# Kernel tuning notes

Hardware: AMD Instinct MI355X
Metric: run time of the kernel (lower is better)

## Reference

```python
import jax, jax.numpy as jnp
import numpy as np

DIM = 768
NUM_HEADS = 12
HEAD_DIM = DIM // NUM_HEADS
SCALE = HEAD_DIM ** -0.5
B, N = 8, 1024


def setup_inputs() -> dict:
    key = jax.random.key(0)
    k1, k2, k3, k4, k5 = jax.random.split(key, 5)
    x = jax.random.normal(k1, (B, N, DIM), dtype=jnp.float32)
    # qkv: Linear(dim, 3*dim, bias=False); proj: Linear(dim, dim) with bias
    w_qkv = jax.random.normal(k2, (3 * DIM, DIM), dtype=jnp.float32) * (DIM ** -0.5)
    w_proj = jax.random.normal(k3, (DIM, DIM), dtype=jnp.float32) * (DIM ** -0.5)
    b_proj = jnp.zeros((DIM,), dtype=jnp.float32)
    # learned attention mask parameter, shape (H, L, L) with L >= N
    att_mask = jax.random.normal(k4, (NUM_HEADS, N, N), dtype=jnp.float32)
    return {"x": x, "w_qkv": w_qkv, "w_proj": w_proj, "b_proj": b_proj, "att_mask": att_mask}


def reference(x, w_qkv, w_proj, b_proj, att_mask):
    Bx, Nx, C = x.shape
    # qkv projection -> (3, B, H, N, head_dim)
    qkv = (x @ w_qkv.T).reshape(Bx, Nx, 3, NUM_HEADS, C // NUM_HEADS)
    qkv = jnp.transpose(qkv, (2, 0, 3, 1, 4))
    q, k, v = qkv[0], qkv[1], qkv[2]  # gpd_ratio==active_ratio==1 -> scaling factor 1
    # scores [B, H, N, N]
    attn = jnp.einsum('bhnd,bhmd->bhnm', q, k) * SCALE
    # custom sigmoid mask gating before softmax (broadcast over batch)
    attn = attn * jax.nn.sigmoid(att_mask[:, :Nx, :Nx])[None, :, :, :]
    attn = jax.nn.softmax(attn, axis=-1)
    out = jnp.einsum('bhnm,bhmd->bhnd', attn, v)
    out = jnp.transpose(out, (0, 2, 1, 3)).reshape(Bx, Nx, C)
    return out @ w_proj.T + b_proj
```

## Files before the change

kernel.cpp:

```cpp
#include <hip/hip_runtime.h>
#include <math.h>
#include <stdint.h>

typedef unsigned short u16;
typedef __attribute__((ext_vector_type(8))) short short8;
typedef __attribute__((ext_vector_type(4))) float f32x4;

#define GATE_SCALE 0.18033688011112042f

#if __has_builtin(__builtin_amdgcn_exp2f)
#define FEXP2(x) __builtin_amdgcn_exp2f(x)
#else
#define FEXP2(x) exp2f(x)
#endif

__device__ __forceinline__ u16 f2b(float f) {
    union { float f; unsigned u; } v; v.f = f;
    unsigned r = v.u + 0x7fffu + ((v.u >> 16) & 1u);
    return (u16)(r >> 16);
}
__device__ __forceinline__ u16 f2b_hu(float f) {
    union { float f; unsigned u; } v; v.f = f;
    return (u16)((v.u + 0x8000u) >> 16);
}
__device__ __forceinline__ float b2f(u16 u) {
    union { float f; unsigned u; } v; v.u = ((unsigned)u) << 16; return v.f;
}

#define GLL16(gsrc, ldsbase) __builtin_amdgcn_global_load_lds(                    \
    (__attribute__((address_space(1))) void*)(uintptr_t)(gsrc),                   \
    (__attribute__((address_space(3))) void*)(uint32_t)(uintptr_t)(ldsbase),      \
    16, 0, 0)

#define NX4  1572864
#define NW14 442368
#define NW24 147456
#define NXW4 (NX4 + NW14 + NW24)

__global__ __launch_bounds__(256) void prep_xw(
    const float4* __restrict__ x, const float4* __restrict__ wq,
    const float4* __restrict__ wp,
    ushort4* __restrict__ xb, ushort4* __restrict__ wqb,
    ushort4* __restrict__ wpb)
{
    size_t i = (size_t)blockIdx.x * 256 + threadIdx.x;
    float4 v; ushort4* dst; size_t j;
    if (i < NX4)            { j = i;               v = x[j];  dst = xb;  }
    else if (i < NX4 + NW14){ j = i - NX4;         v = wq[j]; dst = wqb; }
    else                    { j = i - (NX4 + NW14);v = wp[j]; dst = wpb; }
    ushort4 o; o.x = f2b(v.x); o.y = f2b(v.y); o.z = f2b(v.z); o.w = f2b(v.w);
    dst[j] = o;
}

__global__ __launch_bounds__(256) void prep_gate(
    const float* __restrict__ mask, u16* __restrict__ gp)
{
    const int bid = blockIdx.x;
    const int h = bid >> 8, qt = (bid >> 4) & 15, kt = bid & 15;
    const int t = threadIdx.x, l = t & 63, w = t >> 6;
    const int fq = l >> 4, fr = l & 15;
    const float* mb = mask + ((size_t)h * 1024 + qt * 64 + 16 * w + 4 * fq) * 1024
                           + kt * 64 + fr;
    union { u16 u[16]; float4 f[2]; } vals;
    #pragma unroll
    for (int i = 0; i < 4; ++i)
        #pragma unroll
        for (int nt = 0; nt < 4; ++nt) {
            float m = mb[(size_t)i * 1024 + nt * 16];
            vals.u[i * 4 + nt] = f2b(GATE_SCALE / (1.f + __expf(-m)));
        }
    float4* dst = (float4*)(gp + (size_t)bid * 4096 + (w * 64 + l) * 16);
    dst[0] = vals.f[0];
    dst[1] = vals.f[1];
}

__global__ __launch_bounds__(256) void qkv_gemm(
    const u16* __restrict__ xb, const u16* __restrict__ wb,
    u16* __restrict__ qb, u16* __restrict__ kb, u16* __restrict__ vb)
{
    __shared__ u16 As[2][4096];
    __shared__ u16 Bs[2][4096];
    const int t = threadIdx.x, l = t & 63, w = t >> 6;
    const int wm = (w & 1) * 64, wn = (w >> 1) * 64;
    const int m0 = blockIdx.y * 128, c0 = blockIdx.x * 128;

    f32x4 acc[4][4];
    #pragma unroll
    for (int i = 0; i < 4; ++i)
        #pragma unroll
        for (int j = 0; j < 4; ++j) { f32x4 z = {0.f,0.f,0.f,0.f}; acc[i][j] = z; }

    const int srow = l >> 2, sseg = l & 3;
    const int gcol = ((sseg ^ (srow & 3)) << 3);
    const u16* a0 = xb + (size_t)(m0 + w * 16 + srow) * 768 + gcol;
    const u16* a1 = a0 + (size_t)64 * 768;
    const u16* b0p = wb + (size_t)(c0 + w * 16 + srow) * 768 + gcol;
    const u16* b1p = b0p + (size_t)64 * 768;
    const int wofs = w * 512;

    const int fr = l & 15, fq = l >> 4;
    const int fseg = (fq ^ (fr & 3)) << 3;

    GLL16(a0, &As[0][wofs]);
    GLL16(a1, &As[0][2048 + wofs]);
    GLL16(b0p, &Bs[0][wofs]);
    GLL16(b1p, &Bs[0][2048 + wofs]);

    for (int kt = 0; kt < 24; ++kt) {
        __syncthreads();
        if (kt < 23) {
            const int kn = (kt + 1) * 32;
            const int nb = (kt + 1) & 1;
            GLL16(a0 + kn, &As[nb][wofs]);
            GLL16(a1 + kn, &As[nb][2048 + wofs]);
            GLL16(b0p + kn, &Bs[nb][wofs]);
            GLL16(b1p + kn, &Bs[nb][2048 + wofs]);
        }
        const u16* A = As[kt & 1];
        const u16* B = Bs[kt & 1];
        short8 af[4], bf[4];
        #pragma unroll
        for (int mt = 0; mt < 4; ++mt)
            af[mt] = *(const short8*)&A[(wm + mt * 16 + fr) * 32 + fseg];
        #pragma unroll
        for (int nt = 0; nt < 4; ++nt)
            bf[nt] = *(const short8*)&B[(wn + nt * 16 + fr) * 32 + fseg];
        #pragma unroll
        for (int mt = 0; mt < 4; ++mt)
            #pragma unroll
            for (int nt = 0; nt < 4; ++nt)
                acc[mt][nt] = __builtin_amdgcn_mfma_f32_16x16x32_bf16(
                    af[mt], bf[nt], acc[mt][nt], 0, 0, 0);
    }

    const int b = m0 >> 10;
    const int n0 = m0 & 1023;
    #pragma unroll
    for (int nt = 0; nt < 4; ++nt) {
        const int c = c0 + wn + nt * 16 + fr;
        const int which = c / 768;
        const int rem = c - which * 768;
        const int h = rem >> 6, d = rem & 63;
        if (which < 2) {
            u16* dst = ((which == 0) ? qb : kb)
                       + ((size_t)(b * 12 + h) * 1024) * 64 + d;
            #pragma unroll
            for (int mt = 0; mt < 4; ++mt)
                #pragma unroll
                for (int r = 0; r < 4; ++r) {
                    const int n = n0 + wm + mt * 16 + fq * 4 + r;
                    dst[(size_t)n * 64] = f2b(acc[mt][nt][r]);
                }
        } else {
            u16* dst = vb + ((size_t)(b * 12 + h) * 64 + d) * 1024
                          + n0 + wm + fq * 4;
            #pragma unroll
            for (int mt = 0; mt < 4; ++mt) {
                ushort4 pk;
                pk.x = f2b(acc[mt][nt][0]); pk.y = f2b(acc[mt][nt][1]);
                pk.z = f2b(acc[mt][nt][2]); pk.w = f2b(acc[mt][nt][3]);
                *(ushort4*)(dst + mt * 16) = pk;
            }
        }
    }
}

__global__ __launch_bounds__(256) void flash_attn(
    const u16* __restrict__ qb, const u16* __restrict__ kb,
    const u16* __restrict__ vt, const u16* __restrict__ gperm,
    u16* __restrict__ aob)
{
    __shared__ u16 Qs[4096], Ks[2][4096], Vts[2][4096], Ps[4096];
    const int t = threadIdx.x, l = t & 63, w = t >> 6;
    const int bid = blockIdx.x;
    const int h = bid >> 7, qt = (bid >> 3) & 15, b = bid & 7;
    const int q0 = qt * 64;
    const u16* hq = qb + (size_t)(b * 12 + h) * 65536;
    const u16* hk = kb + (size_t)(b * 12 + h) * 65536;
    const u16* hv = vt + (size_t)(b * 12 + h) * 65536;
    const u16* hg = gperm + (size_t)(h * 256 + qt * 16) * 4096 + (w * 64 + l) * 16;

    const int sr = l >> 3, ss = l & 7;
    const int sg = ((ss ^ (sr & 7)) << 3);
    const int j0 = w * 2, j1 = w * 2 + 1;

    GLL16(hq + (size_t)(q0 + j0 * 8 + sr) * 64 + sg, Qs + j0 * 512);
    GLL16(hq + (size_t)(q0 + j1 * 8 + sr) * 64 + sg, Qs + j1 * 512);
    GLL16(hk + (size_t)(j0 * 8 + sr) * 64 + sg, &Ks[0][j0 * 512]);
    GLL16(hk + (size_t)(j1 * 8 + sr) * 64 + sg, &Ks[0][j1 * 512]);
    GLL16(hv + (size_t)(j0 * 8 + sr) * 1024 + sg, &Vts[0][j0 * 512]);
    GLL16(hv + (size_t)(j1 * 8 + sr) * 1024 + sg, &Vts[0][j1 * 512]);

    short8 g0 = *(const short8*)(hg);
    short8 g1 = *(const short8*)(hg + 8);

    float l_part[4] = {0.f, 0.f, 0.f, 0.f};
    f32x4 o[4];
    #pragma unroll
    for (int nt = 0; nt < 4; ++nt) { f32x4 z = {0.f,0.f,0.f,0.f}; o[nt] = z; }

    const int fq = l >> 4, fr = l & 15;
    const int sega = ((fq ^ (fr & 7)) << 3);
    const int segb = (((4 + fq) ^ (fr & 7)) << 3);

    for (int kt = 0; kt < 16; ++kt) {
        __syncthreads();
        if (kt < 15) {
            const int nb = (kt + 1) & 1;
            const size_t ko = (size_t)(kt + 1) * 64;
            GLL16(hk + (ko + j0 * 8 + sr) * 64 + sg, &Ks[nb][j0 * 512]);
            GLL16(hk + (ko + j1 * 8 + sr) * 64 + sg, &Ks[nb][j1 * 512]);
            GLL16(hv + (size_t)(j0 * 8 + sr) * 1024 + ko + sg, &Vts[nb][j0 * 512]);
            GLL16(hv + (size_t)(j1 * 8 + sr) * 1024 + ko + sg, &Vts[nb][j1 * 512]);
        }
        const int ktn = (kt < 15) ? kt + 1 : 15;
        short8 gn0 = *(const short8*)(hg + (size_t)ktn * 4096);
        short8 gn1 = *(const short8*)(hg + (size_t)ktn * 4096 + 8);

        const u16* Kc = Ks[kt & 1];
        const u16* Vc = Vts[kt & 1];

        short8 aq0 = *(const short8*)&Qs[(16 * w + fr) * 64 + sega];
        short8 aq1 = *(const short8*)&Qs[(16 * w + fr) * 64 + segb];
        f32x4 sv[4];
        #pragma unroll
        for (int nt = 0; nt < 4; ++nt) {
            short8 k0f = *(const short8*)&Kc[(nt * 16 + fr) * 64 + sega];
            short8 k1f = *(const short8*)&Kc[(nt * 16 + fr) * 64 + segb];
            f32x4 z = {0.f,0.f,0.f,0.f};
            z = __builtin_amdgcn_mfma_f32_16x16x32_bf16(aq0, k0f, z, 0, 0, 0);
            z = __builtin_amdgcn_mfma_f32_16x16x32_bf16(aq1, k1f, z, 0, 0, 0);
            sv[nt] = z;
        }

        #pragma unroll
        for (int i = 0; i < 4; ++i) {
            const int pr = 4 * fq + i;
            #pragma unroll
            for (int nt = 0; nt < 4; ++nt) {
                const int idx = i * 4 + nt;
                const float g = b2f((u16)(idx < 8 ? g0[idx] : g1[idx - 8]));
                const float p = FEXP2(sv[nt][i] * g);
                l_part[i] += p;
                const int col = nt * 16 + fr;
                Ps[w * 1024 + pr * 64 + (((col >> 3) ^ (pr & 7)) << 3) + (col & 7)]
                    = f2b_hu(p);
            }
        }

        short8 ap0 = *(const short8*)&Ps[w * 1024 + fr * 64 + sega];
        short8 ap1 = *(const short8*)&Ps[w * 1024 + fr * 64 + segb];
        #pragma unroll
        for (int nt = 0; nt < 4; ++nt) {
            short8 v0 = *(const short8*)&Vc[(nt * 16 + fr) * 64 + sega];
            short8 v1 = *(const short8*)&Vc[(nt * 16 + fr) * 64 + segb];
            o[nt] = __builtin_amdgcn_mfma_f32_16x16x32_bf16(ap0, v0, o[nt], 0, 0, 0);
            o[nt] = __builtin_amdgcn_mfma_f32_16x16x32_bf16(ap1, v1, o[nt], 0, 0, 0);
        }

        g0 = gn0;
        g1 = gn1;
    }

    float l_i[4];
    #pragma unroll
    for (int i = 0; i < 4; ++i) {
        float s = l_part[i];
        s += __shfl_xor(s, 1, 16);
        s += __shfl_xor(s, 2, 16);
        s += __shfl_xor(s, 4, 16);
        s += __shfl_xor(s, 8, 16);
        l_i[i] = s;
    }

    #pragma unroll
    for (int i = 0; i < 4; ++i) {
        const float inv = 1.f / l_i[i];
        const int n = q0 + 16 * w + 4 * fq + i;
        const size_t rowoff = ((size_t)b * 1024 + n) * 768 + h * 64;
        #pragma unroll
        for (int nt = 0; nt < 4; ++nt)
            aob[rowoff + nt * 16 + fr] = f2b(o[nt][i] * inv);
    }
}

__global__ __launch_bounds__(256) void proj_gemm(
    const u16* __restrict__ aob, const u16* __restrict__ wb,
    const float* __restrict__ bproj, float* __restrict__ out)
{
    __shared__ u16 As[2][4096];
    __shared__ u16 Bs[2][4096];
    const int t = threadIdx.x, l = t & 63, w = t >> 6;
    const int wm = (w & 1) * 64, wn = (w >> 1) * 64;
    const int m0 = blockIdx.y * 128, c0 = blockIdx.x * 128;

    f32x4 acc[4][4];
    #pragma unroll
    for (int i = 0; i < 4; ++i)
        #pragma unroll
        for (int j = 0; j < 4; ++j) { f32x4 z = {0.f,0.f,0.f,0.f}; acc[i][j] = z; }

    const int srow = l >> 2, sseg = l & 3;
    const int gcol = ((sseg ^ (srow & 3)) << 3);
    const u16* a0 = aob + (size_t)(m0 + w * 16 + srow) * 768 + gcol;
    const u16* a1 = a0 + (size_t)64 * 768;
    const u16* b0p = wb + (size_t)(c0 + w * 16 + srow) * 768 + gcol;
    const u16* b1p = b0p + (size_t)64 * 768;
    const int wofs = w * 512;

    const int fr = l & 15, fq = l >> 4;
    const int fseg = (fq ^ (fr & 3)) << 3;

    GLL16(a0, &As[0][wofs]);
    GLL16(a1, &As[0][2048 + wofs]);
    GLL16(b0p, &Bs[0][wofs]);
    GLL16(b1p, &Bs[0][2048 + wofs]);

    for (int kt = 0; kt < 24; ++kt) {
        __syncthreads();
        if (kt < 23) {
            const int kn = (kt + 1) * 32;
            const int nb = (kt + 1) & 1;
            GLL16(a0 + kn, &As[nb][wofs]);
            GLL16(a1 + kn, &As[nb][2048 + wofs]);
            GLL16(b0p + kn, &Bs[nb][wofs]);
            GLL16(b1p + kn, &Bs[nb][2048 + wofs]);
        }
        const u16* A = As[kt & 1];
        const u16* B = Bs[kt & 1];
        short8 af[4], bf[4];
        #pragma unroll
        for (int mt = 0; mt < 4; ++mt)
            af[mt] = *(const short8*)&A[(wm + mt * 16 + fr) * 32 + fseg];
        #pragma unroll
        for (int nt = 0; nt < 4; ++nt)
            bf[nt] = *(const short8*)&B[(wn + nt * 16 + fr) * 32 + fseg];
        #pragma unroll
        for (int mt = 0; mt < 4; ++mt)
            #pragma unroll
            for (int nt = 0; nt < 4; ++nt)
                acc[mt][nt] = __builtin_amdgcn_mfma_f32_16x16x32_bf16(
                    af[mt], bf[nt], acc[mt][nt], 0, 0, 0);
    }

    #pragma unroll
    for (int nt = 0; nt < 4; ++nt) {
        const int c = c0 + wn + nt * 16 + fr;
        const float bias = bproj[c];
        #pragma unroll
        for (int mt = 0; mt < 4; ++mt)
            #pragma unroll
            for (int r = 0; r < 4; ++r) {
                const int m = m0 + wm + mt * 16 + fq * 4 + r;
                out[(size_t)m * 768 + c] = acc[mt][nt][r] + bias;
            }
    }
}

extern "C" void kernel_launch(void* const* d_in, const int* in_sizes, int n_in,
                              void* d_out, int out_size, void* d_ws, size_t ws_size,
                              hipStream_t stream)
{
    const float* x     = (const float*)d_in[0];
    const float* wqkv  = (const float*)d_in[1];
    const float* wproj = (const float*)d_in[2];
    const float* bproj = (const float*)d_in[3];
    const float* mask  = (const float*)d_in[4];
    float* out = (float*)d_out;

    char* ws = (char*)d_ws;
    u16* gperm  = (u16*)(ws);
    u16* xb     = (u16*)(ws + 25165824);
    u16* wqkvb  = (u16*)(ws + 37748736);
    u16* wprojb = (u16*)(ws + 41287680);
    u16* qb     = (u16*)(ws + 42467328);
    u16* kb     = (u16*)(ws + 55050240);
    u16* vb     = (u16*)(ws + 67633152);
    u16* aob    = (u16*)(ws + 80216064);

    prep_xw<<<NXW4 / 256, 256, 0, stream>>>(
        (const float4*)x, (const float4*)wqkv, (const float4*)wproj,
        (ushort4*)xb, (ushort4*)wqkvb, (ushort4*)wprojb);

    prep_gate<<<3072, 256, 0, stream>>>(mask, gperm);

    qkv_gemm<<<dim3(18, 64), 256, 0, stream>>>(xb, wqkvb, qb, kb, vb);

    flash_attn<<<1536, 256, 0, stream>>>(qb, kb, vb, gperm, aob);

    proj_gemm<<<dim3(6, 64), 256, 0, stream>>>(aob, wprojb, bproj, out);
}
```

Before: 249.1 us.

## Use 32x32x16 MFMA with 128-row query tiles in flash attention

The attention kernel now gives each block 128 query rows, so each wave owns 32 rows. It uses 32x32x16 bf16 MFMA instructions in place of 16x16x32, and keeps Q fragments in registers for the whole loop. The gate-permutation prep kernel is rewritten to match the new fragment layout. K/V double buffering is removed in favour of a single buffer with two barriers per iteration, and the kernel sets launch bounds for 3 blocks per CU. This halves the K/V reloads per query and uses larger MFMAs, at the cost of less load/compute overlap and higher register pressure.

```diff
diff --git a/kernel.cpp b/kernel.cpp
--- a/kernel.cpp
+++ b/kernel.cpp
@@ -5,6 +5,7 @@
 typedef unsigned short u16;
 typedef __attribute__((ext_vector_type(8))) short short8;
 typedef __attribute__((ext_vector_type(4))) float f32x4;
+typedef __attribute__((ext_vector_type(16))) float f32x16;
 
 #define GATE_SCALE 0.18033688011112042f
 
@@ -56,22 +57,22 @@
     const float* __restrict__ mask, u16* __restrict__ gp)
 {
     const int bid = blockIdx.x;
-    const int h = bid >> 8, qt = (bid >> 4) & 15, kt = bid & 15;
+    const int kt = bid & 15, qt = (bid >> 4) & 7, h = bid >> 7;
     const int t = threadIdx.x, l = t & 63, w = t >> 6;
-    const int fq = l >> 4, fr = l & 15;
-    const float* mb = mask + ((size_t)h * 1024 + qt * 64 + 16 * w + 4 * fq) * 1024
-                           + kt * 64 + fr;
-    union { u16 u[16]; float4 f[2]; } vals;
-    #pragma unroll
-    for (int i = 0; i < 4; ++i)
-        #pragma unroll
-        for (int nt = 0; nt < 4; ++nt) {
-            float m = mb[(size_t)i * 1024 + nt * 16];
-            vals.u[i * 4 + nt] = f2b(GATE_SCALE / (1.f + __expf(-m)));
-        }
-    float4* dst = (float4*)(gp + (size_t)bid * 4096 + (w * 64 + l) * 16);
-    dst[0] = vals.f[0];
-    dst[1] = vals.f[1];
+    const int ln = l & 31, lh = l >> 5;
+    union { u16 u[32]; float4 f[4]; } vals;
+    #pragma unroll
+    for (int ktile = 0; ktile < 2; ++ktile)
+        #pragma unroll
+        for (int reg = 0; reg < 16; ++reg) {
+            const int q   = qt * 128 + 32 * w + (reg & 3) + 8 * (reg >> 2) + 4 * lh;
+            const int key = kt * 64 + ktile * 32 + ln;
+            const float m = mask[((size_t)h * 1024 + q) * 1024 + key];
+            vals.u[ktile * 16 + reg] = f2b(GATE_SCALE / (1.f + __expf(-m)));
+        }
+    float4* dst = (float4*)(gp + (size_t)bid * 8192 + (w * 64 + l) * 32);
+    #pragma unroll
+    for (int s = 0; s < 4; ++s) dst[s] = vals.f[s];
 }
 
 __global__ __launch_bounds__(256) void qkv_gemm(
@@ -165,122 +166,142 @@
     }
 }
 
-__global__ __launch_bounds__(256) void flash_attn(
+__global__ __launch_bounds__(256, 3) void flash_attn(
     const u16* __restrict__ qb, const u16* __restrict__ kb,
     const u16* __restrict__ vt, const u16* __restrict__ gperm,
     u16* __restrict__ aob)
 {
-    __shared__ u16 Qs[4096], Ks[2][4096], Vts[2][4096], Ps[4096];
+    __shared__ u16 Qs[8192];
+    __shared__ u16 Ks[4096];
+    __shared__ u16 Vts[4096];
+    __shared__ u16 Ps[8192];
+
     const int t = threadIdx.x, l = t & 63, w = t >> 6;
+    const int ln = l & 31, lh = l >> 5;
     const int bid = blockIdx.x;
-    const int h = bid >> 7, qt = (bid >> 3) & 15, b = bid & 7;
-    const int q0 = qt * 64;
-    const u16* hq = qb + (size_t)(b * 12 + h) * 65536;
-    const u16* hk = kb + (size_t)(b * 12 + h) * 65536;
-    const u16* hv = vt + (size_t)(b * 12 + h) * 65536;
-    const u16* hg = gperm + (size_t)(h * 256 + qt * 16) * 4096 + (w * 64 + l) * 16;
+    const int qt = bid & 7, bh = bid >> 3;
+    const int h = bh % 12, b = bh / 12;
+    const int q0 = qt * 128;
+
+    const u16* hq = qb + (size_t)bh * 65536;
+    const u16* hk = kb + (size_t)bh * 65536;
+    const u16* hv = vt + (size_t)bh * 65536;
+    const u16* hg = gperm + ((size_t)(h * 8 + qt) * 16) * 8192 + (w * 64 + l) * 32;
 
     const int sr = l >> 3, ss = l & 7;
     const int sg = ((ss ^ (sr & 7)) << 3);
-    const int j0 = w * 2, j1 = w * 2 + 1;
-
-    GLL16(hq + (size_t)(q0 + j0 * 8 + sr) * 64 + sg, Qs + j0 * 512);
-    GLL16(hq + (size_t)(q0 + j1 * 8 + sr) * 64 + sg, Qs + j1 * 512);
-    GLL16(hk + (size_t)(j0 * 8 + sr) * 64 + sg, &Ks[0][j0 * 512]);
-    GLL16(hk + (size_t)(j1 * 8 + sr) * 64 + sg, &Ks[0][j1 * 512]);
-    GLL16(hv + (size_t)(j0 * 8 + sr) * 1024 + sg, &Vts[0][j0 * 512]);
-    GLL16(hv + (size_t)(j1 * 8 + sr) * 1024 + sg, &Vts[0][j1 * 512]);
-
-    short8 g0 = *(const short8*)(hg);
-    short8 g1 = *(const short8*)(hg + 8);
-
-    float l_part[4] = {0.f, 0.f, 0.f, 0.f};
-    f32x4 o[4];
-    #pragma unroll
-    for (int nt = 0; nt < 4; ++nt) { f32x4 z = {0.f,0.f,0.f,0.f}; o[nt] = z; }
-
-    const int fq = l >> 4, fr = l & 15;
-    const int sega = ((fq ^ (fr & 7)) << 3);
-    const int segb = (((4 + fq) ^ (fr & 7)) << 3);
+
+    #pragma unroll
+    for (int jq = 0; jq < 4; ++jq) {
+        const int j = w * 4 + jq;
+        GLL16(hq + (size_t)(q0 + j * 8 + sr) * 64 + sg, Qs + j * 512);
+    }
+    {
+        const int j0 = w * 2, j1 = w * 2 + 1;
+        GLL16(hk + (size_t)(j0 * 8 + sr) * 64 + sg, Ks + j0 * 512);
+        GLL16(hk + (size_t)(j1 * 8 + sr) * 64 + sg, Ks + j1 * 512);
+        GLL16(hv + (size_t)(j0 * 8 + sr) * 1024 + sg, Vts + j0 * 512);
+        GLL16(hv + (size_t)(j1 * 8 + sr) * 1024 + sg, Vts + j1 * 512);
+    }
+    __syncthreads();
+
+    short8 aq[4];
+    {
+        const int qrow = 32 * w + ln;
+        #pragma unroll
+        for (int kd = 0; kd < 4; ++kd)
+            aq[kd] = *(const short8*)&Qs[qrow * 64 + ((((kd << 1) | lh) ^ (qrow & 7)) << 3)];
+    }
+
+    float l_part[16];
+    #pragma unroll
+    for (int r = 0; r < 16; ++r) l_part[r] = 0.f;
+    f32x16 o[2];
+    #pragma unroll
+    for (int dt = 0; dt < 2; ++dt)
+        #pragma unroll
+        for (int r = 0; r < 16; ++r) o[dt][r] = 0.f;
 
     for (int kt = 0; kt < 16; ++kt) {
-        __syncthreads();
-        if (kt < 15) {
-            const int nb = (kt + 1) & 1;
-            const size_t ko = (size_t)(kt + 1) * 64;
-            GLL16(hk + (ko + j0 * 8 + sr) * 64 + sg, &Ks[nb][j0 * 512]);
-            GLL16(hk + (ko + j1 * 8 + sr) * 64 + sg, &Ks[nb][j1 * 512]);
-            GLL16(hv + (size_t)(j0 * 8 + sr) * 1024 + ko + sg, &Vts[nb][j0 * 512]);
-            GLL16(hv + (size_t)(j1 * 8 + sr) * 1024 + ko + sg, &Vts[nb][j1 * 512]);
-        }
-        const int ktn = (kt < 15) ? kt + 1 : 15;
-        short8 gn0 = *(const short8*)(hg + (size_t)ktn * 4096);
-        short8 gn1 = *(const short8*)(hg + (size_t)ktn * 4096 + 8);
-
-        const u16* Kc = Ks[kt & 1];
-        const u16* Vc = Vts[kt & 1];
-
-        short8 aq0 = *(const short8*)&Qs[(16 * w + fr) * 64 + sega];
-        short8 aq1 = *(const short8*)&Qs[(16 * w + fr) * 64 + segb];
-        f32x4 sv[4];
-        #pragma unroll
-        for (int nt = 0; nt < 4; ++nt) {
-            short8 k0f = *(const short8*)&Kc[(nt * 16 + fr) * 64 + sega];
-            short8 k1f = *(const short8*)&Kc[(nt * 16 + fr) * 64 + segb];
-            f32x4 z = {0.f,0.f,0.f,0.f};
-            z = __builtin_amdgcn_mfma_f32_16x16x32_bf16(aq0, k0f, z, 0, 0, 0);
-            z = __builtin_amdgcn_mfma_f32_16x16x32_bf16(aq1, k1f, z, 0, 0, 0);
-            sv[nt] = z;
-        }
-
-        #pragma unroll
-        for (int i = 0; i < 4; ++i) {
-            const int pr = 4 * fq + i;
-            #pragma unroll
-            for (int nt = 0; nt < 4; ++nt) {
-                const int idx = i * 4 + nt;
-                const float g = b2f((u16)(idx < 8 ? g0[idx] : g1[idx - 8]));
-                const float p = FEXP2(sv[nt][i] * g);
-                l_part[i] += p;
-                const int col = nt * 16 + fr;
-                Ps[w * 1024 + pr * 64 + (((col >> 3) ^ (pr & 7)) << 3) + (col & 7)]
+        short8 g[4];
+        #pragma unroll
+        for (int s = 0; s < 4; ++s)
+            g[s] = *(const short8*)(hg + (size_t)kt * 8192 + s * 8);
+
+        f32x16 sv[2];
+        #pragma unroll
+        for (int ktile = 0; ktile < 2; ++ktile) {
+            f32x16 z;
+            #pragma unroll
+            for (int r = 0; r < 16; ++r) z[r] = 0.f;
+            #pragma unroll
+            for (int kd = 0; kd < 4; ++kd) {
+                const int krow = ktile * 32 + ln;
+                short8 bk = *(const short8*)&Ks[krow * 64 + ((((kd << 1) | lh) ^ (krow & 7)) << 3)];
+                z = __builtin_amdgcn_mfma_f32_32x32x16_bf16(aq[kd], bk, z, 0, 0, 0);
+            }
+            sv[ktile] = z;
+        }
+
+        #pragma unroll
+        for (int ktile = 0; ktile < 2; ++ktile)
+            #pragma unroll
+            for (int reg = 0; reg < 16; ++reg) {
+                const int idx = ktile * 16 + reg;
+                const float gv = b2f((u16)g[idx >> 3][idx & 7]);
+                const float p = FEXP2(sv[ktile][reg] * gv);
+                l_part[reg] += p;
+                const int qr = (reg & 3) + 8 * (reg >> 2) + 4 * lh;
+                const int col = ktile * 32 + ln;
+                Ps[w * 2048 + qr * 64 + (((col >> 3) ^ (qr & 7)) << 3) + (col & 7)]
                     = f2b_hu(p);
             }
-        }
-
-        short8 ap0 = *(const short8*)&Ps[w * 1024 + fr * 64 + sega];
-        short8 ap1 = *(const short8*)&Ps[w * 1024 + fr * 64 + segb];
-        #pragma unroll
-        for (int nt = 0; nt < 4; ++nt) {
-            short8 v0 = *(const short8*)&Vc[(nt * 16 + fr) * 64 + sega];
-            short8 v1 = *(const short8*)&Vc[(nt * 16 + fr) * 64 + segb];
-            o[nt] = __builtin_amdgcn_mfma_f32_16x16x32_bf16(ap0, v0, o[nt], 0, 0, 0);
-            o[nt] = __builtin_amdgcn_mfma_f32_16x16x32_bf16(ap1, v1, o[nt], 0, 0, 0);
-        }
-
-        g0 = gn0;
-        g1 = gn1;
-    }
-
-    float l_i[4];
-    #pragma unroll
-    for (int i = 0; i < 4; ++i) {
-        float s = l_part[i];
-        s += __shfl_xor(s, 1, 16);
-        s += __shfl_xor(s, 2, 16);
-        s += __shfl_xor(s, 4, 16);
-        s += __shfl_xor(s, 8, 16);
-        l_i[i] = s;
-    }
-
-    #pragma unroll
-    for (int i = 0; i < 4; ++i) {
-        const float inv = 1.f / l_i[i];
-        const int n = q0 + 16 * w + 4 * fq + i;
-        const size_t rowoff = ((size_t)b * 1024 + n) * 768 + h * 64;
-        #pragma unroll
-        for (int nt = 0; nt < 4; ++nt)
-            aob[rowoff + nt * 16 + fr] = f2b(o[nt][i] * inv);
+
+        short8 ap[4];
+        #pragma unroll
+        for (int kp = 0; kp < 4; ++kp)
+            ap[kp] = *(const short8*)&Ps[w * 2048 + ln * 64 + ((((kp << 1) | lh) ^ (ln & 7)) << 3)];
+        #pragma unroll
+        for (int dt = 0; dt < 2; ++dt) {
+            #pragma unroll
+            for (int kp = 0; kp < 4; ++kp) {
+                const int drow = dt * 32 + ln;
+                short8 bv = *(const short8*)&Vts[drow * 64 + ((((kp << 1) | lh) ^ (drow & 7)) << 3)];
+                o[dt] = __builtin_amdgcn_mfma_f32_32x32x16_bf16(ap[kp], bv, o[dt], 0, 0, 0);
+            }
+        }
+
+        if (kt < 15) {
+            __syncthreads();
+            const int j0 = w * 2, j1 = w * 2 + 1;
+            const size_t ko = (size_t)(kt + 1) * 64;
+            GLL16(hk + (ko + j0 * 8 + sr) * 64 + sg, Ks + j0 * 512);
+            GLL16(hk + (ko + j1 * 8 + sr) * 64 + sg, Ks + j1 * 512);
+            GLL16(hv + (size_t)(j0 * 8 + sr) * 1024 + ko + sg, Vts + j0 * 512);
+            GLL16(hv + (size_t)(j1 * 8 + sr) * 1024 + ko + sg, Vts + j1 * 512);
+            __syncthreads();
+        }
+    }
+
+    float inv[16];
+    #pragma unroll
+    for (int reg = 0; reg < 16; ++reg) {
+        float s = l_part[reg];
+        s += __shfl_xor(s, 1, 32);
+        s += __shfl_xor(s, 2, 32);
+        s += __shfl_xor(s, 4, 32);
+        s += __shfl_xor(s, 8, 32);
+        s += __shfl_xor(s, 16, 32);
+        inv[reg] = 1.f / s;
+    }
+
+    #pragma unroll
+    for (int reg = 0; reg < 16; ++reg) {
+        const int qr = (reg & 3) + 8 * (reg >> 2) + 4 * lh;
+        const int n = q0 + 32 * w + qr;
+        u16* dst = aob + ((size_t)b * 1024 + n) * 768 + h * 64 + ln;
+        dst[0]  = f2b(o[0][reg] * inv[reg]);
+        dst[32] = f2b(o[1][reg] * inv[reg]);
     }
 }
 
@@ -382,11 +403,11 @@
         (const float4*)x, (const float4*)wqkv, (const float4*)wproj,
         (ushort4*)xb, (ushort4*)wqkvb, (ushort4*)wprojb);
 
-    prep_gate<<<3072, 256, 0, stream>>>(mask, gperm);
+    prep_gate<<<1536, 256, 0, stream>>>(mask, gperm);
 
     qkv_gemm<<<dim3(18, 64), 256, 0, stream>>>(xb, wqkvb, qb, kb, vb);
 
-    flash_attn<<<1536, 256, 0, stream>>>(qb, kb, vb, gperm, aob);
+    flash_attn<<<768, 256, 0, stream>>>(qb, kb, vb, gperm, aob);
 
     proj_gemm<<<dim3(6, 64), 256, 0, stream>>>(aob, wprojb, bproj, out);
 }
```

Measured after the change: 305.3 us. +22.5%, slower.

## Double query tile per attention block and coalesce gate prep via LDS transpose

Applied to the files above, without the earlier changes.

Each flash_attn block now processes 128 query rows (two 64-row halves) against every K/V tile, so K/V loads from global memory and LDS are shared across twice as many queries, which halves the grid. K/V double buffering is removed in favour of single buffers with two barriers around each reload, and launch bounds now request 3 blocks per CU. prep_gate reads the mask with coalesced float4 loads into a padded LDS tile and then writes the permuted layout, replacing strided scalar reads. The cost is more registers per thread, loads that are no longer overlapped with MFMA work, and fewer blocks to fill the GPU.

```diff
diff --git a/kernel.cpp b/kernel.cpp
--- a/kernel.cpp
+++ b/kernel.cpp
@@ -53,23 +53,34 @@
 }
 
 __global__ __launch_bounds__(256) void prep_gate(
-    const float* __restrict__ mask, u16* __restrict__ gp)
-{
+    const float4* __restrict__ mask4, u16* __restrict__ gp)
+{
+    __shared__ u16 L[64][72];
     const int bid = blockIdx.x;
-    const int h = bid >> 8, qt = (bid >> 4) & 15, kt = bid & 15;
-    const int t = threadIdx.x, l = t & 63, w = t >> 6;
+    const int kt = bid & 15, qt = (bid >> 4) & 15, h = bid >> 8;
+    const int t = threadIdx.x;
+
+    #pragma unroll
+    for (int s = 0; s < 4; ++s) {
+        const int idx = t + s * 256;
+        const int row = idx >> 4, c4 = idx & 15;
+        float4 v = mask4[(size_t)(h * 1024 + qt * 64 + row) * 256 + kt * 16 + c4];
+        L[row][c4 * 4 + 0] = f2b(GATE_SCALE / (1.f + __expf(-v.x)));
+        L[row][c4 * 4 + 1] = f2b(GATE_SCALE / (1.f + __expf(-v.y)));
+        L[row][c4 * 4 + 2] = f2b(GATE_SCALE / (1.f + __expf(-v.z)));
+        L[row][c4 * 4 + 3] = f2b(GATE_SCALE / (1.f + __expf(-v.w)));
+    }
+    __syncthreads();
+
+    const int w = t >> 6, l = t & 63;
     const int fq = l >> 4, fr = l & 15;
-    const float* mb = mask + ((size_t)h * 1024 + qt * 64 + 16 * w + 4 * fq) * 1024
-                           + kt * 64 + fr;
     union { u16 u[16]; float4 f[2]; } vals;
     #pragma unroll
     for (int i = 0; i < 4; ++i)
         #pragma unroll
-        for (int nt = 0; nt < 4; ++nt) {
-            float m = mb[(size_t)i * 1024 + nt * 16];
-            vals.u[i * 4 + nt] = f2b(GATE_SCALE / (1.f + __expf(-m)));
-        }
-    float4* dst = (float4*)(gp + (size_t)bid * 4096 + (w * 64 + l) * 16);
+        for (int nt = 0; nt < 4; ++nt)
+            vals.u[i * 4 + nt] = L[16 * w + 4 * fq + i][nt * 16 + fr];
+    float4* dst = (float4*)(gp + (size_t)bid * 4096 + (size_t)t * 16);
     dst[0] = vals.f[0];
     dst[1] = vals.f[1];
 }
@@ -165,122 +176,149 @@
     }
 }
 
-__global__ __launch_bounds__(256) void flash_attn(
+__global__ __launch_bounds__(256, 3) void flash_attn(
     const u16* __restrict__ qb, const u16* __restrict__ kb,
     const u16* __restrict__ vt, const u16* __restrict__ gperm,
     u16* __restrict__ aob)
 {
-    __shared__ u16 Qs[4096], Ks[2][4096], Vts[2][4096], Ps[4096];
+    __shared__ u16 Qs[8192], Ks[4096], Vts[4096], Ps[4096];
     const int t = threadIdx.x, l = t & 63, w = t >> 6;
     const int bid = blockIdx.x;
-    const int h = bid >> 7, qt = (bid >> 3) & 15, b = bid & 7;
-    const int q0 = qt * 64;
-    const u16* hq = qb + (size_t)(b * 12 + h) * 65536;
-    const u16* hk = kb + (size_t)(b * 12 + h) * 65536;
-    const u16* hv = vt + (size_t)(b * 12 + h) * 65536;
-    const u16* hg = gperm + (size_t)(h * 256 + qt * 16) * 4096 + (w * 64 + l) * 16;
+    const int qtb = bid & 7, bh = bid >> 3;
+    const int h = bh % 12, b = bh / 12;
+    const int q0 = qtb * 128;
+
+    const u16* hq = qb + (size_t)bh * 65536;
+    const u16* hk = kb + (size_t)bh * 65536;
+    const u16* hv = vt + (size_t)bh * 65536;
+    const u16* hgb = gperm + ((size_t)h * 256 + qtb * 32) * 4096 + (w * 64 + l) * 16;
 
     const int sr = l >> 3, ss = l & 7;
     const int sg = ((ss ^ (sr & 7)) << 3);
-    const int j0 = w * 2, j1 = w * 2 + 1;
-
-    GLL16(hq + (size_t)(q0 + j0 * 8 + sr) * 64 + sg, Qs + j0 * 512);
-    GLL16(hq + (size_t)(q0 + j1 * 8 + sr) * 64 + sg, Qs + j1 * 512);
-    GLL16(hk + (size_t)(j0 * 8 + sr) * 64 + sg, &Ks[0][j0 * 512]);
-    GLL16(hk + (size_t)(j1 * 8 + sr) * 64 + sg, &Ks[0][j1 * 512]);
-    GLL16(hv + (size_t)(j0 * 8 + sr) * 1024 + sg, &Vts[0][j0 * 512]);
-    GLL16(hv + (size_t)(j1 * 8 + sr) * 1024 + sg, &Vts[0][j1 * 512]);
-
-    short8 g0 = *(const short8*)(hg);
-    short8 g1 = *(const short8*)(hg + 8);
-
-    float l_part[4] = {0.f, 0.f, 0.f, 0.f};
-    f32x4 o[4];
-    #pragma unroll
-    for (int nt = 0; nt < 4; ++nt) { f32x4 z = {0.f,0.f,0.f,0.f}; o[nt] = z; }
+    const int j0 = w * 2, j1 = j0 + 1;
+
+    #pragma unroll
+    for (int jq = 0; jq < 4; ++jq) {
+        const int j = w * 4 + jq;
+        GLL16(hq + (size_t)(q0 + j * 8 + sr) * 64 + sg, Qs + j * 512);
+    }
+    GLL16(hk + (size_t)(j0 * 8 + sr) * 64 + sg, Ks + j0 * 512);
+    GLL16(hk + (size_t)(j1 * 8 + sr) * 64 + sg, Ks + j1 * 512);
+    GLL16(hv + (size_t)(j0 * 8 + sr) * 1024 + sg, Vts + j0 * 512);
+    GLL16(hv + (size_t)(j1 * 8 + sr) * 1024 + sg, Vts + j1 * 512);
+    __syncthreads();
 
     const int fq = l >> 4, fr = l & 15;
     const int sega = ((fq ^ (fr & 7)) << 3);
     const int segb = (((4 + fq) ^ (fr & 7)) << 3);
 
+    short8 aq[2][2];
+    #pragma unroll
+    for (int qh = 0; qh < 2; ++qh) {
+        const int row = 16 * w + fr;
+        aq[qh][0] = *(const short8*)&Qs[qh * 4096 + row * 64 + sega];
+        aq[qh][1] = *(const short8*)&Qs[qh * 4096 + row * 64 + segb];
+    }
+
+    short8 gn[4];
+    gn[0] = *(const short8*)(hgb);
+    gn[1] = *(const short8*)(hgb + 8);
+    gn[2] = *(const short8*)(hgb + 65536);
+    gn[3] = *(const short8*)(hgb + 65536 + 8);
+
+    float l_part[2][4] = {{0.f,0.f,0.f,0.f},{0.f,0.f,0.f,0.f}};
+    f32x4 o[2][4];
+    #pragma unroll
+    for (int qh = 0; qh < 2; ++qh)
+        #pragma unroll
+        for (int nt = 0; nt < 4; ++nt) { f32x4 z = {0.f,0.f,0.f,0.f}; o[qh][nt] = z; }
+
     for (int kt = 0; kt < 16; ++kt) {
-        __syncthreads();
+        short8 g[4];
+        #pragma unroll
+        for (int s = 0; s < 4; ++s) g[s] = gn[s];
         if (kt < 15) {
-            const int nb = (kt + 1) & 1;
+            const size_t go = (size_t)(kt + 1) * 4096;
+            gn[0] = *(const short8*)(hgb + go);
+            gn[1] = *(const short8*)(hgb + go + 8);
+            gn[2] = *(const short8*)(hgb + 65536 + go);
+            gn[3] = *(const short8*)(hgb + 65536 + go + 8);
+        }
+
+        f32x4 sv[2][4];
+        #pragma unroll
+        for (int nt = 0; nt < 4; ++nt) {
+            short8 kf0 = *(const short8*)&Ks[(nt * 16 + fr) * 64 + sega];
+            short8 kf1 = *(const short8*)&Ks[(nt * 16 + fr) * 64 + segb];
+            f32x4 z0 = {0.f,0.f,0.f,0.f};
+            z0 = __builtin_amdgcn_mfma_f32_16x16x32_bf16(aq[0][0], kf0, z0, 0, 0, 0);
+            z0 = __builtin_amdgcn_mfma_f32_16x16x32_bf16(aq[0][1], kf1, z0, 0, 0, 0);
+            sv[0][nt] = z0;
+            f32x4 z1 = {0.f,0.f,0.f,0.f};
+            z1 = __builtin_amdgcn_mfma_f32_16x16x32_bf16(aq[1][0], kf0, z1, 0, 0, 0);
+            z1 = __builtin_amdgcn_mfma_f32_16x16x32_bf16(aq[1][1], kf1, z1, 0, 0, 0);
+            sv[1][nt] = z1;
+        }
+
+        short8 ap[2][2];
+        #pragma unroll
+        for (int qh = 0; qh < 2; ++qh) {
+            #pragma unroll
+            for (int i = 0; i < 4; ++i) {
+                const int pr = 4 * fq + i;
+                #pragma unroll
+                for (int nt = 0; nt < 4; ++nt) {
+                    const int idx = i * 4 + nt;
+                    const float gv = b2f((u16)(idx < 8 ? g[2 * qh][idx]
+                                                       : g[2 * qh + 1][idx - 8]));
+                    const float p = FEXP2(sv[qh][nt][i] * gv);
+                    l_part[qh][i] += p;
+                    const int col = nt * 16 + fr;
+                    Ps[w * 1024 + pr * 64 + (((col >> 3) ^ (pr & 7)) << 3) + (col & 7)]
+                        = f2b_hu(p);
+                }
+            }
+            ap[qh][0] = *(const short8*)&Ps[w * 1024 + fr * 64 + sega];
+            ap[qh][1] = *(const short8*)&Ps[w * 1024 + fr * 64 + segb];
+        }
+
+        #pragma unroll
+        for (int nt = 0; nt < 4; ++nt) {
+            short8 vf0 = *(const short8*)&Vts[(nt * 16 + fr) * 64 + sega];
+            short8 vf1 = *(const short8*)&Vts[(nt * 16 + fr) * 64 + segb];
+            o[0][nt] = __builtin_amdgcn_mfma_f32_16x16x32_bf16(ap[0][0], vf0, o[0][nt], 0, 0, 0);
+            o[0][nt] = __builtin_amdgcn_mfma_f32_16x16x32_bf16(ap[0][1], vf1, o[0][nt], 0, 0, 0);
+            o[1][nt] = __builtin_amdgcn_mfma_f32_16x16x32_bf16(ap[1][0], vf0, o[1][nt], 0, 0, 0);
+            o[1][nt] = __builtin_amdgcn_mfma_f32_16x16x32_bf16(ap[1][1], vf1, o[1][nt], 0, 0, 0);
+        }
+
+        if (kt < 15) {
+            __syncthreads();
             const size_t ko = (size_t)(kt + 1) * 64;
-            GLL16(hk + (ko + j0 * 8 + sr) * 64 + sg, &Ks[nb][j0 * 512]);
-            GLL16(hk + (ko + j1 * 8 + sr) * 64 + sg, &Ks[nb][j1 * 512]);
-            GLL16(hv + (size_t)(j0 * 8 + sr) * 1024 + ko + sg, &Vts[nb][j0 * 512]);
-            GLL16(hv + (size_t)(j1 * 8 + sr) * 1024 + ko + sg, &Vts[nb][j1 * 512]);
-        }
-        const int ktn = (kt < 15) ? kt + 1 : 15;
-        short8 gn0 = *(const short8*)(hg + (size_t)ktn * 4096);
-        short8 gn1 = *(const short8*)(hg + (size_t)ktn * 4096 + 8);
-
-        const u16* Kc = Ks[kt & 1];
-        const u16* Vc = Vts[kt & 1];
-
-        short8 aq0 = *(const short8*)&Qs[(16 * w + fr) * 64 + sega];
-        short8 aq1 = *(const short8*)&Qs[(16 * w + fr) * 64 + segb];
-        f32x4 sv[4];
-        #pragma unroll
-        for (int nt = 0; nt < 4; ++nt) {
-            short8 k0f = *(const short8*)&Kc[(nt * 16 + fr) * 64 + sega];
-            short8 k1f = *(const short8*)&Kc[(nt * 16 + fr) * 64 + segb];
-            f32x4 z = {0.f,0.f,0.f,0.f};
-            z = __builtin_amdgcn_mfma_f32_16x16x32_bf16(aq0, k0f, z, 0, 0, 0);
-            z = __builtin_amdgcn_mfma_f32_16x16x32_bf16(aq1, k1f, z, 0, 0, 0);
-            sv[nt] = z;
-        }
-
+            GLL16(hk + (ko + j0 * 8 + sr) * 64 + sg, Ks + j0 * 512);
+            GLL16(hk + (ko + j1 * 8 + sr) * 64 + sg, Ks + j1 * 512);
+            GLL16(hv + (size_t)(j0 * 8 + sr) * 1024 + ko + sg, Vts + j0 * 512);
+            GLL16(hv + (size_t)(j1 * 8 + sr) * 1024 + ko + sg, Vts + j1 * 512);
+            __syncthreads();
+        }
+    }
+
+    #pragma unroll
+    for (int qh = 0; qh < 2; ++qh) {
         #pragma unroll
         for (int i = 0; i < 4; ++i) {
-            const int pr = 4 * fq + i;
-            #pragma unroll
-            for (int nt = 0; nt < 4; ++nt) {
-                const int idx = i * 4 + nt;
-                const float g = b2f((u16)(idx < 8 ? g0[idx] : g1[idx - 8]));
-                const float p = FEXP2(sv[nt][i] * g);
-                l_part[i] += p;
-                const int col = nt * 16 + fr;
-                Ps[w * 1024 + pr * 64 + (((col >> 3) ^ (pr & 7)) << 3) + (col & 7)]
-                    = f2b_hu(p);
-            }
-        }
-
-        short8 ap0 = *(const short8*)&Ps[w * 1024 + fr * 64 + sega];
-        short8 ap1 = *(const short8*)&Ps[w * 1024 + fr * 64 + segb];
-        #pragma unroll
-        for (int nt = 0; nt < 4; ++nt) {
-            short8 v0 = *(const short8*)&Vc[(nt * 16 + fr) * 64 + sega];
-            short8 v1 = *(const short8*)&Vc[(nt * 16 + fr) * 64 + segb];
-            o[nt] = __builtin_amdgcn_mfma_f32_16x16x32_bf16(ap0, v0, o[nt], 0, 0, 0);
-            o[nt] = __builtin_amdgcn_mfma_f32_16x16x32_bf16(ap1, v1, o[nt], 0, 0, 0);
-        }
-
-        g0 = gn0;
-        g1 = gn1;
-    }
-
-    float l_i[4];
-    #pragma unroll
-    for (int i = 0; i < 4; ++i) {
-        float s = l_part[i];
-        s += __shfl_xor(s, 1, 16);
-        s += __shfl_xor(s, 2, 16);
-        s += __shfl_xor(s, 4, 16);
-        s += __shfl_xor(s, 8, 16);
-        l_i[i] = s;
-    }
-
-    #pragma unroll
-    for (int i = 0; i < 4; ++i) {
-        const float inv = 1.f / l_i[i];
-        const int n = q0 + 16 * w + 4 * fq + i;
-        const size_t rowoff = ((size_t)b * 1024 + n) * 768 + h * 64;
-        #pragma unroll
-        for (int nt = 0; nt < 4; ++nt)
-            aob[rowoff + nt * 16 + fr] = f2b(o[nt][i] * inv);
+            float s = l_part[qh][i];
+            s += __shfl_xor(s, 1, 16);
+            s += __shfl_xor(s, 2, 16);
+            s += __shfl_xor(s, 4, 16);
+            s += __shfl_xor(s, 8, 16);
+            const float inv = 1.f / s;
+            const int n = q0 + qh * 64 + 16 * w + 4 * fq + i;
+            const size_t rowoff = ((size_t)b * 1024 + n) * 768 + h * 64;
+            #pragma unroll
+            for (int nt = 0; nt < 4; ++nt)
+                aob[rowoff + nt * 16 + fr] = f2b(o[qh][nt][i] * inv);
+        }
     }
 }
 
@@ -382,11 +420,11 @@
         (const float4*)x, (const float4*)wqkv, (const float4*)wproj,
         (ushort4*)xb, (ushort4*)wqkvb, (ushort4*)wprojb);
 
-    prep_gate<<<3072, 256, 0, stream>>>(mask, gperm);
+    prep_gate<<<3072, 256, 0, stream>>>((const float4*)mask, gperm);
 
     qkv_gemm<<<dim3(18, 64), 256, 0, stream>>>(xb, wqkvb, qb, kb, vb);
 
-    flash_attn<<<1536, 256, 0, stream>>>(qb, kb, vb, gperm, aob);
+    flash_attn<<<768, 256, 0, stream>>>(qb, kb, vb, gperm, aob);
 
     proj_gemm<<<dim3(6, 64), 256, 0, stream>>>(aob, wprojb, bproj, out);
 }
```

Result: faster. 243.7 us (-2.2%).
